# Optimization experiments

Measured on AMD Instinct MI355X. Metric: run time of the kernel, lower is better.

## Reference

```python
import jax, jax.numpy as jnp
import numpy as np

RGB2GRAY = jnp.array([0.299, 0.587, 0.114], dtype=jnp.float32)


def _trilinear_slice(grid, z, y, x):
    """grid: (F, L, GH, GW); z,y,x: (H, W) float positions in index space
    (align_corners=True convention). Returns (H, W, F)."""
    F_, L, GH, GW = grid.shape
    z = jnp.clip(z, 0.0, L - 1)
    y = jnp.clip(y, 0.0, GH - 1)
    x = jnp.clip(x, 0.0, GW - 1)
    z0 = jnp.floor(z).astype(jnp.int32); z1 = jnp.minimum(z0 + 1, L - 1)
    y0 = jnp.floor(y).astype(jnp.int32); y1 = jnp.minimum(y0 + 1, GH - 1)
    x0 = jnp.floor(x).astype(jnp.int32); x1 = jnp.minimum(x0 + 1, GW - 1)
    wz = (z - z0)[..., None]  # (H, W, 1)
    wy = (y - y0)[..., None]
    wx = (x - x0)[..., None]

    def g(zi, yi, xi):  # gather corner -> (H, W, F)
        return jnp.moveaxis(grid[:, zi, yi, xi], 0, -1)

    c00 = g(z0, y0, x0) * (1 - wx) + g(z0, y0, x1) * wx
    c01 = g(z0, y1, x0) * (1 - wx) + g(z0, y1, x1) * wx
    c10 = g(z1, y0, x0) * (1 - wx) + g(z1, y0, x1) * wx
    c11 = g(z1, y1, x0) * (1 - wx) + g(z1, y1, x1) * wx
    c0 = c00 * (1 - wy) + c01 * wy
    c1 = c10 * (1 - wy) + c11 * wy
    return c0 * (1 - wz) + c1 * wz


def setup_inputs() -> dict:
    key = jax.random.key(0)
    k = jax.random.split(key, 5)
    H, W = 1080, 1920
    N, F_, L, GH, GW = 50, 16, 8, 16, 16
    hidden = 64
    rgb = jax.random.uniform(k[0], (H, W, 3), dtype=jnp.float32)
    grids = jax.random.normal(k[1], (N, F_, L, GH, GW), dtype=jnp.float32) * 0.1
    W1 = jax.random.normal(k[2], (hidden, F_), dtype=jnp.float32) * (1.0 / np.sqrt(F_))
    W2 = jax.random.normal(k[3], (hidden, hidden), dtype=jnp.float32) * (1.0 / np.sqrt(hidden))
    W3 = jax.random.normal(k[4], (12, hidden), dtype=jnp.float32) * (1.0 / np.sqrt(hidden))
    return {"rgb": rgb, "grids": grids, "W1": W1, "W2": W2, "W3": W3, "cam_idx": 3}


def reference(rgb, grids, W1, W2, W3, cam_idx):
    H, W, _ = rgb.shape
    _, F_, L, GH, GW = grids.shape
    grid = grids[cam_idx]  # (F, L, GH, GW)
    # guidance: gray in [0,1]; grid_sample coords in [-1,1] with align_corners=True
    # map directly to index space: pos = coord01 * (size - 1)
    gray = jnp.clip(jnp.tensordot(rgb, RGB2GRAY, axes=([-1], [0])), 0.0, 1.0)  # (H, W)
    gy = jnp.linspace(0.0, 1.0, H, dtype=jnp.float32)[:, None]  # (H, 1)
    gx = jnp.linspace(0.0, 1.0, W, dtype=jnp.float32)[None, :]  # (1, W)
    z = gray * (L - 1)
    y = jnp.broadcast_to(gy * (GH - 1), (H, W))
    x = jnp.broadcast_to(gx * (GW - 1), (H, W))
    feat = _trilinear_slice(grid, z, y, x)  # (H, W, F)
    # tiny per-pixel MLP (bias-free, torch Linear applies x @ W.T)
    h = jnp.tanh(feat @ W1.T)
    h = jnp.tanh(h @ W2.T)
    out = h @ W3.T  # (H, W, 12)
    return out.reshape(1, H, W, 3, 4)
```

## Files before the change

### kernel.cpp

```cpp
#include <hip/hip_runtime.h>

#define H_IMG 1080
#define W_IMG 1920
#define NPIX (H_IMG * W_IMG)

typedef __attribute__((ext_vector_type(8))) short bfrag8;
typedef __attribute__((ext_vector_type(4))) float facc4;

#define PK2_OFF 131072
#define PK3_OFF 147456
#define PK1_OFF 151552

__device__ __forceinline__ void split_bf16(float x, unsigned short& hi, unsigned short& lo) {
    unsigned xu = __float_as_uint(x);
    hi = (unsigned short)(xu >> 16);
    float hif = __uint_as_float(xu & 0xffff0000u);
    float lof = x - hif;
    lo = (unsigned short)(__float_as_uint(lof) >> 16);
}

__global__ void prep_kernel(const float* __restrict__ grids,
                            const int* __restrict__ cam_idx,
                            const float* __restrict__ W1,
                            const float* __restrict__ W2,
                            const float* __restrict__ W3,
                            float* __restrict__ grid_t,
                            unsigned short* __restrict__ pk1,
                            unsigned short* __restrict__ pk2,
                            unsigned short* __restrict__ pk3) {
    int idx = blockIdx.x * 256 + threadIdx.x;
    {
        int f = idx & 15, x = (idx >> 4) & 15, y = (idx >> 8) & 15, z = (idx >> 12) & 7;
        int cam = cam_idx[0];
        grid_t[idx] = grids[(((cam * 16 + f) * 8 + z) * 16 + y) * 16 + x];
    }
    if (idx < 8192) {
        int i = idx & 7, lane = (idx >> 3) & 63, h = (idx >> 9) & 1,
            s = (idx >> 10) & 1, mt = (idx >> 11) & 3;
        int j = mt * 16 + (lane & 15);
        int k = s * 32 + (lane >> 4) * 8 + i;
        unsigned short hi, lo;
        split_bf16(W2[j * 64 + k], hi, lo);
        pk2[idx] = h ? lo : hi;
    } else if (idx < 10240) {
        int e = idx - 8192;
        int i = e & 7, lane = (e >> 3) & 63, h = (e >> 9) & 1, s = (e >> 10) & 1;
        int c = lane & 15;
        int k = s * 32 + (lane >> 4) * 8 + i;
        float x = (c < 12) ? W3[c * 64 + k] : 0.0f;
        unsigned short hi, lo;
        split_bf16(x, hi, lo);
        pk3[e] = h ? lo : hi;
    } else if (idx < 14336) {
        int e = idx - 10240;
        int i = e & 7, lane = (e >> 3) & 63, h = (e >> 9) & 1, mt = (e >> 10) & 3;
        int j = mt * 16 + (lane & 15);
        int k = (lane >> 4) * 8 + i;
        float x = (k < 16) ? W1[j * 16 + k] : 0.0f;
        unsigned short hi, lo;
        split_bf16(x, hi, lo);
        pk1[e] = h ? lo : hi;
    }
}

__device__ __forceinline__ float fast_tanh(float x) {
    float e = exp2f(x * 2.8853900817779268f);
    return 1.0f - 2.0f * __builtin_amdgcn_rcpf(e + 1.0f);
}

__device__ __forceinline__ unsigned pack_hi_pair(float e, float o) {
    return __builtin_amdgcn_perm(__float_as_uint(o), __float_as_uint(e), 0x07060302u);
}

#define DS_FENCE() asm volatile("s_waitcnt lgkmcnt(0)" ::: "memory")
#define MFMA16(A, B, C) __builtin_amdgcn_mfma_f32_16x16x32_bf16((A), (B), (C), 0, 0, 0)

__global__ __launch_bounds__(256, 3)
void nbat_main(const float* __restrict__ rgb,
               const float* __restrict__ grid_t,
               const unsigned short* __restrict__ pk1,
               const unsigned short* __restrict__ pk2,
               const unsigned short* __restrict__ pk3,
               float* __restrict__ out) {
    __shared__ __align__(16) unsigned hbuf[4][2048];

    const int tid = threadIdx.x;
    const int w = tid >> 6, l = tid & 63;
    const int g = l >> 4, cc = l & 15;
    unsigned* hb = hbuf[w];
    uint4* hb4 = (uint4*)hb;

    const int pixbase = blockIdx.x * 256 + w * 64;
    const int pix = pixbase + l;
    const int row = pix / W_IMG;
    const int col = pix - row * W_IMG;

    float r = rgb[3 * pix + 0];
    float gch = rgb[3 * pix + 1];
    float b = rgb[3 * pix + 2];
    float gray = fminf(fmaxf(0.299f * r + 0.587f * gch + 0.114f * b, 0.0f), 1.0f);

    float z = fminf(fmaxf(gray * 7.0f, 0.0f), 7.0f);
    float y = (float)row * (15.0f / 1079.0f);
    float x = (float)col * (15.0f / 1919.0f);

    float zf = floorf(z), yf = floorf(y), xf = floorf(x);
    int z0 = (int)zf, y0 = (int)yf, x0 = (int)xf;
    int z1 = min(z0 + 1, 7), y1 = min(y0 + 1, 15), x1 = min(x0 + 1, 15);
    float wz = z - zf, wy = y - yf, wx = x - xf;

    float feat[16];
#pragma unroll
    for (int i = 0; i < 16; ++i) feat[i] = 0.0f;

    const float4* gt4 = (const float4*)grid_t;
#pragma unroll
    for (int cz = 0; cz < 2; ++cz) {
        int zz = cz ? z1 : z0;
        float wwz = cz ? wz : (1.0f - wz);
#pragma unroll
        for (int cy = 0; cy < 2; ++cy) {
            int yy = cy ? y1 : y0;
            float wwzy = wwz * (cy ? wy : (1.0f - wy));
#pragma unroll
            for (int cx = 0; cx < 2; ++cx) {
                int xx = cx ? x1 : x0;
                float wc = wwzy * (cx ? wx : (1.0f - wx));
                int base = ((zz * 16 + yy) * 16 + xx) * 4;
#pragma unroll
                for (int q = 0; q < 4; ++q) {
                    float4 v = gt4[base + q];
                    feat[4 * q + 0] = fmaf(wc, v.x, feat[4 * q + 0]);
                    feat[4 * q + 1] = fmaf(wc, v.y, feat[4 * q + 1]);
                    feat[4 * q + 2] = fmaf(wc, v.z, feat[4 * q + 2]);
                    feat[4 * q + 3] = fmaf(wc, v.w, feat[4 * q + 3]);
                }
            }
        }
    }

    const int sl = (l >> 1) & 3;
    {
        uint4 q0, q1;
        q0.x = pack_hi_pair(feat[0], feat[1]);
        q0.y = pack_hi_pair(feat[2], feat[3]);
        q0.z = pack_hi_pair(feat[4], feat[5]);
        q0.w = pack_hi_pair(feat[6], feat[7]);
        q1.x = pack_hi_pair(feat[8], feat[9]);
        q1.y = pack_hi_pair(feat[10], feat[11]);
        q1.z = pack_hi_pair(feat[12], feat[13]);
        q1.w = pack_hi_pair(feat[14], feat[15]);
        uint4 zz4 = make_uint4(0u, 0u, 0u, 0u);
        hb4[l * 4 + (0 ^ sl)] = q0;
        hb4[l * 4 + (1 ^ sl)] = q1;
        hb4[l * 4 + (2 ^ sl)] = zz4;
        hb4[l * 4 + (3 ^ sl)] = zz4;
    }
    DS_FENCE();

    bfrag8 bf[4];
#pragma unroll
    for (int nt = 0; nt < 4; ++nt) {
        int p = cc + 16 * nt;
        bf[nt] = __builtin_bit_cast(bfrag8, hb4[p * 4 + (g ^ ((p >> 1) & 3))]);
    }
    DS_FENCE();

    auto transition = [&](const facc4& v, int mtl, int nt) __attribute__((always_inline)) {
        float t0 = fast_tanh(v[0]);
        float t1 = fast_tanh(v[1]);
        float t2 = fast_tanh(v[2]);
        float t3 = fast_tanh(v[3]);
        unsigned hA = pack_hi_pair(t0, t1);
        unsigned hB = pack_hi_pair(t2, t3);
        float l0 = t0 - __uint_as_float(hA << 16);
        float l1 = t1 - __uint_as_float(hA & 0xffff0000u);
        float l2 = t2 - __uint_as_float(hB << 16);
        float l3 = t3 - __uint_as_float(hB & 0xffff0000u);
        unsigned lA = pack_hi_pair(l0, l1);
        unsigned lB = pack_hi_pair(l2, l3);
        int p = cc + 16 * nt;
        int u = p * 16 + ((((mtl << 1) + (g >> 1)) ^ ((p >> 1) & 3)) << 2) + ((g & 1) << 1);
        *(uint2*)(hb + u) = make_uint2(hA, hB);
        *(uint2*)(hb + 1024 + u) = make_uint2(lA, lB);
    };

    const bfrag8* pk1v = (const bfrag8*)pk1;
    const bfrag8* pk2v = (const bfrag8*)pk2;

    facc4 acc2[4][4];
#pragma unroll
    for (int mt = 0; mt < 4; ++mt)
#pragma unroll
        for (int nt = 0; nt < 4; ++nt) acc2[mt][nt] = (facc4){0.f, 0.f, 0.f, 0.f};

#pragma unroll
    for (int s = 0; s < 2; ++s) {
        facc4 a1[2][4];
#pragma unroll
        for (int mtl = 0; mtl < 2; ++mtl)
#pragma unroll
            for (int nt = 0; nt < 4; ++nt) a1[mtl][nt] = (facc4){0.f, 0.f, 0.f, 0.f};
#pragma unroll
        for (int mtl = 0; mtl < 2; ++mtl) {
            int mt = 2 * s + mtl;
            bfrag8 w1h = pk1v[(mt * 2 + 0) * 64 + l];
            bfrag8 w1l = pk1v[(mt * 2 + 1) * 64 + l];
#pragma unroll
            for (int nt = 0; nt < 4; ++nt) {
                a1[mtl][nt] = MFMA16(w1l, bf[nt], a1[mtl][nt]);
                a1[mtl][nt] = MFMA16(w1h, bf[nt], a1[mtl][nt]);
            }
        }
#pragma unroll
        for (int mtl = 0; mtl < 2; ++mtl)
#pragma unroll
            for (int nt = 0; nt < 4; ++nt) transition(a1[mtl][nt], mtl, nt);
        DS_FENCE();
        bfrag8 w2h[4], w2l[4];
#pragma unroll
        for (int mt = 0; mt < 4; ++mt) {
            w2h[mt] = pk2v[((mt * 2 + s) * 2 + 0) * 64 + l];
            w2l[mt] = pk2v[((mt * 2 + s) * 2 + 1) * 64 + l];
        }
#pragma unroll
        for (int nt = 0; nt < 4; ++nt) {
            int p = cc + 16 * nt;
            int sw = (p >> 1) & 3;
            uint4 qh = hb4[p * 4 + (g ^ sw)];
            uint4 ql = hb4[256 + p * 4 + (g ^ sw)];
            bfrag8 bh = __builtin_bit_cast(bfrag8, qh);
            bfrag8 bl = __builtin_bit_cast(bfrag8, ql);
#pragma unroll
            for (int mt = 0; mt < 4; ++mt) {
                acc2[mt][nt] = MFMA16(w2h[mt], bl, acc2[mt][nt]);
                acc2[mt][nt] = MFMA16(w2l[mt], bh, acc2[mt][nt]);
                acc2[mt][nt] = MFMA16(w2h[mt], bh, acc2[mt][nt]);
            }
        }
        DS_FENCE();
    }

    const bfrag8* pk3v = (const bfrag8*)pk3;
    facc4 o3[4];
#pragma unroll
    for (int nt = 0; nt < 4; ++nt) o3[nt] = (facc4){0.f, 0.f, 0.f, 0.f};

#pragma unroll
    for (int s = 0; s < 2; ++s) {
#pragma unroll
        for (int mtl = 0; mtl < 2; ++mtl)
#pragma unroll
            for (int nt = 0; nt < 4; ++nt) transition(acc2[2 * s + mtl][nt], mtl, nt);
        DS_FENCE();
        bfrag8 w3h = pk3v[(s * 2 + 0) * 64 + l];
        bfrag8 w3l = pk3v[(s * 2 + 1) * 64 + l];
#pragma unroll
        for (int nt = 0; nt < 4; ++nt) {
            int p = cc + 16 * nt;
            int sw = (p >> 1) & 3;
            uint4 qh = hb4[p * 4 + (g ^ sw)];
            uint4 ql = hb4[256 + p * 4 + (g ^ sw)];
            bfrag8 bh = __builtin_bit_cast(bfrag8, qh);
            bfrag8 bl = __builtin_bit_cast(bfrag8, ql);
            o3[nt] = MFMA16(w3h, bl, o3[nt]);
            o3[nt] = MFMA16(w3l, bh, o3[nt]);
            o3[nt] = MFMA16(w3h, bh, o3[nt]);
        }
        if (s == 0) DS_FENCE();
    }

    if (g < 3) {
#pragma unroll
        for (int nt = 0; nt < 4; ++nt) {
            int p = pixbase + 16 * nt + cc;
            *(float4*)(out + p * 12 + 4 * g) =
                make_float4(o3[nt][0], o3[nt][1], o3[nt][2], o3[nt][3]);
        }
    }
}

extern "C" void kernel_launch(void* const* d_in, const int* in_sizes, int n_in,
                              void* d_out, int out_size, void* d_ws, size_t ws_size,
                              hipStream_t stream) {
    const float* rgb   = (const float*)d_in[0];
    const float* grids = (const float*)d_in[1];
    const float* W1    = (const float*)d_in[2];
    const float* W2    = (const float*)d_in[3];
    const float* W3    = (const float*)d_in[4];
    const int*   cam   = (const int*)d_in[5];

    float* grid_t = (float*)d_ws;
    unsigned short* pk2 = (unsigned short*)((char*)d_ws + PK2_OFF);
    unsigned short* pk3 = (unsigned short*)((char*)d_ws + PK3_OFF);
    unsigned short* pk1 = (unsigned short*)((char*)d_ws + PK1_OFF);

    hipLaunchKernelGGL(prep_kernel, dim3(128), dim3(256), 0, stream,
                       grids, cam, W1, W2, W3, grid_t, pk1, pk2, pk3);
    hipLaunchKernelGGL(nbat_main, dim3(NPIX / 256), dim3(256), 0, stream,
                       rgb, grid_t, pk1, pk2, pk3, (float*)d_out);
}
```

Baseline: 176.8 us.

## Drop hi/lo split of activations, round-to-nearest bf16, full-layer staging

Activations in layers 2 and 3 are now a single round-to-nearest bf16 value instead of a hi+lo bf16 pair. This cuts MFMAs per layer from 3 to 2 per tile and removes the low-part LDS traffic. Layer 1 is now computed in full before one transition, with the LDS swizzle simplified and the explicit lgkmcnt waits replaced by compiler-only barriers. The risks are lower numerical accuracy in the activations and possible LDS hazards if the compiler does not order the wave-local writes and reads, plus more live registers (acc1 and acc2 full arrays).

```diff
diff --git a/kernel.cpp b/kernel.cpp
--- a/kernel.cpp
+++ b/kernel.cpp
@@ -68,11 +68,13 @@
     return 1.0f - 2.0f * __builtin_amdgcn_rcpf(e + 1.0f);
 }
 
-__device__ __forceinline__ unsigned pack_hi_pair(float e, float o) {
-    return __builtin_amdgcn_perm(__float_as_uint(o), __float_as_uint(e), 0x07060302u);
-}
-
-#define DS_FENCE() asm volatile("s_waitcnt lgkmcnt(0)" ::: "memory")
+__device__ __forceinline__ unsigned rtn_pair(float e, float o) {
+    unsigned ue = __float_as_uint(e) + 0x8000u;
+    unsigned uo = __float_as_uint(o) + 0x8000u;
+    return __builtin_amdgcn_perm(uo, ue, 0x07060302u);
+}
+
+#define CBAR() asm volatile("" ::: "memory")
 #define MFMA16(A, B, C) __builtin_amdgcn_mfma_f32_16x16x32_bf16((A), (B), (C), 0, 0, 0)
 
 __global__ __launch_bounds__(256, 3)
@@ -139,135 +141,134 @@
         }
     }
 
-    const int sl = (l >> 1) & 3;
+    const int slw = l & 3;
     {
         uint4 q0, q1;
-        q0.x = pack_hi_pair(feat[0], feat[1]);
-        q0.y = pack_hi_pair(feat[2], feat[3]);
-        q0.z = pack_hi_pair(feat[4], feat[5]);
-        q0.w = pack_hi_pair(feat[6], feat[7]);
-        q1.x = pack_hi_pair(feat[8], feat[9]);
-        q1.y = pack_hi_pair(feat[10], feat[11]);
-        q1.z = pack_hi_pair(feat[12], feat[13]);
-        q1.w = pack_hi_pair(feat[14], feat[15]);
+        q0.x = rtn_pair(feat[0], feat[1]);
+        q0.y = rtn_pair(feat[2], feat[3]);
+        q0.z = rtn_pair(feat[4], feat[5]);
+        q0.w = rtn_pair(feat[6], feat[7]);
+        q1.x = rtn_pair(feat[8], feat[9]);
+        q1.y = rtn_pair(feat[10], feat[11]);
+        q1.z = rtn_pair(feat[12], feat[13]);
+        q1.w = rtn_pair(feat[14], feat[15]);
         uint4 zz4 = make_uint4(0u, 0u, 0u, 0u);
-        hb4[l * 4 + (0 ^ sl)] = q0;
-        hb4[l * 4 + (1 ^ sl)] = q1;
-        hb4[l * 4 + (2 ^ sl)] = zz4;
-        hb4[l * 4 + (3 ^ sl)] = zz4;
-    }
-    DS_FENCE();
+        hb4[l * 4 + (0 ^ slw)] = q0;
+        hb4[l * 4 + (1 ^ slw)] = q1;
+        hb4[l * 4 + (2 ^ slw)] = zz4;
+        hb4[l * 4 + (3 ^ slw)] = zz4;
+    }
+    CBAR();
 
     bfrag8 bf[4];
 #pragma unroll
     for (int nt = 0; nt < 4; ++nt) {
         int p = cc + 16 * nt;
-        bf[nt] = __builtin_bit_cast(bfrag8, hb4[p * 4 + (g ^ ((p >> 1) & 3))]);
-    }
-    DS_FENCE();
-
-    auto transition = [&](const facc4& v, int mtl, int nt) __attribute__((always_inline)) {
+        bf[nt] = __builtin_bit_cast(bfrag8, hb4[p * 4 + (g ^ (p & 3))]);
+    }
+    CBAR();
+
+    auto transition = [&](const facc4& v, int mt, int nt) __attribute__((always_inline)) {
         float t0 = fast_tanh(v[0]);
         float t1 = fast_tanh(v[1]);
         float t2 = fast_tanh(v[2]);
         float t3 = fast_tanh(v[3]);
-        unsigned hA = pack_hi_pair(t0, t1);
-        unsigned hB = pack_hi_pair(t2, t3);
-        float l0 = t0 - __uint_as_float(hA << 16);
-        float l1 = t1 - __uint_as_float(hA & 0xffff0000u);
-        float l2 = t2 - __uint_as_float(hB << 16);
-        float l3 = t3 - __uint_as_float(hB & 0xffff0000u);
-        unsigned lA = pack_hi_pair(l0, l1);
-        unsigned lB = pack_hi_pair(l2, l3);
+        unsigned A = rtn_pair(t0, t1);
+        unsigned B = rtn_pair(t2, t3);
         int p = cc + 16 * nt;
-        int u = p * 16 + ((((mtl << 1) + (g >> 1)) ^ ((p >> 1) & 3)) << 2) + ((g & 1) << 1);
-        *(uint2*)(hb + u) = make_uint2(hA, hB);
-        *(uint2*)(hb + 1024 + u) = make_uint2(lA, lB);
+        int mtl = mt & 1;
+        int c = 2 * mtl + (g >> 1);
+        int u = (mt >> 1) * 1024 + p * 16 + (((c ^ (p & 3)) << 2) + 2 * (g & 1));
+        *(uint2*)(hb + u) = make_uint2(A, B);
     };
 
     const bfrag8* pk1v = (const bfrag8*)pk1;
     const bfrag8* pk2v = (const bfrag8*)pk2;
-
+    const bfrag8* pk3v = (const bfrag8*)pk3;
+
+    facc4 acc1[4][4];
+#pragma unroll
+    for (int mt = 0; mt < 4; ++mt)
+#pragma unroll
+        for (int nt = 0; nt < 4; ++nt) acc1[mt][nt] = (facc4){0.f, 0.f, 0.f, 0.f};
+#pragma unroll
+    for (int mt = 0; mt < 4; ++mt) {
+        bfrag8 w1h = pk1v[(mt * 2 + 0) * 64 + l];
+        bfrag8 w1l = pk1v[(mt * 2 + 1) * 64 + l];
+#pragma unroll
+        for (int nt = 0; nt < 4; ++nt) {
+            acc1[mt][nt] = MFMA16(w1l, bf[nt], acc1[mt][nt]);
+            acc1[mt][nt] = MFMA16(w1h, bf[nt], acc1[mt][nt]);
+        }
+    }
+
+#pragma unroll
+    for (int mt = 0; mt < 4; ++mt)
+#pragma unroll
+        for (int nt = 0; nt < 4; ++nt) transition(acc1[mt][nt], mt, nt);
+    CBAR();
+
+    uint4 Bq[2][4];
+#pragma unroll
+    for (int s = 0; s < 2; ++s)
+#pragma unroll
+        for (int nt = 0; nt < 4; ++nt) {
+            int p = cc + 16 * nt;
+            Bq[s][nt] = hb4[s * 256 + p * 4 + (g ^ (p & 3))];
+        }
     facc4 acc2[4][4];
 #pragma unroll
     for (int mt = 0; mt < 4; ++mt)
 #pragma unroll
         for (int nt = 0; nt < 4; ++nt) acc2[mt][nt] = (facc4){0.f, 0.f, 0.f, 0.f};
-
-#pragma unroll
-    for (int s = 0; s < 2; ++s) {
-        facc4 a1[2][4];
-#pragma unroll
-        for (int mtl = 0; mtl < 2; ++mtl)
-#pragma unroll
-            for (int nt = 0; nt < 4; ++nt) a1[mtl][nt] = (facc4){0.f, 0.f, 0.f, 0.f};
-#pragma unroll
-        for (int mtl = 0; mtl < 2; ++mtl) {
-            int mt = 2 * s + mtl;
-            bfrag8 w1h = pk1v[(mt * 2 + 0) * 64 + l];
-            bfrag8 w1l = pk1v[(mt * 2 + 1) * 64 + l];
-#pragma unroll
-            for (int nt = 0; nt < 4; ++nt) {
-                a1[mtl][nt] = MFMA16(w1l, bf[nt], a1[mtl][nt]);
-                a1[mtl][nt] = MFMA16(w1h, bf[nt], a1[mtl][nt]);
-            }
-        }
-#pragma unroll
-        for (int mtl = 0; mtl < 2; ++mtl)
-#pragma unroll
-            for (int nt = 0; nt < 4; ++nt) transition(a1[mtl][nt], mtl, nt);
-        DS_FENCE();
-        bfrag8 w2h[4], w2l[4];
-#pragma unroll
-        for (int mt = 0; mt < 4; ++mt) {
-            w2h[mt] = pk2v[((mt * 2 + s) * 2 + 0) * 64 + l];
-            w2l[mt] = pk2v[((mt * 2 + s) * 2 + 1) * 64 + l];
-        }
+#pragma unroll
+    for (int mt = 0; mt < 4; ++mt) {
+        bfrag8 w2h0 = pk2v[((mt * 2 + 0) * 2 + 0) * 64 + l];
+        bfrag8 w2l0 = pk2v[((mt * 2 + 0) * 2 + 1) * 64 + l];
+        bfrag8 w2h1 = pk2v[((mt * 2 + 1) * 2 + 0) * 64 + l];
+        bfrag8 w2l1 = pk2v[((mt * 2 + 1) * 2 + 1) * 64 + l];
+#pragma unroll
+        for (int nt = 0; nt < 4; ++nt) {
+            bfrag8 b0 = __builtin_bit_cast(bfrag8, Bq[0][nt]);
+            bfrag8 b1 = __builtin_bit_cast(bfrag8, Bq[1][nt]);
+            acc2[mt][nt] = MFMA16(w2l0, b0, acc2[mt][nt]);
+            acc2[mt][nt] = MFMA16(w2h0, b0, acc2[mt][nt]);
+            acc2[mt][nt] = MFMA16(w2l1, b1, acc2[mt][nt]);
+            acc2[mt][nt] = MFMA16(w2h1, b1, acc2[mt][nt]);
+        }
+    }
+    CBAR();
+
+#pragma unroll
+    for (int mt = 0; mt < 4; ++mt)
+#pragma unroll
+        for (int nt = 0; nt < 4; ++nt) transition(acc2[mt][nt], mt, nt);
+    CBAR();
+
+#pragma unroll
+    for (int s = 0; s < 2; ++s)
 #pragma unroll
         for (int nt = 0; nt < 4; ++nt) {
             int p = cc + 16 * nt;
-            int sw = (p >> 1) & 3;
-            uint4 qh = hb4[p * 4 + (g ^ sw)];
-            uint4 ql = hb4[256 + p * 4 + (g ^ sw)];
-            bfrag8 bh = __builtin_bit_cast(bfrag8, qh);
-            bfrag8 bl = __builtin_bit_cast(bfrag8, ql);
-#pragma unroll
-            for (int mt = 0; mt < 4; ++mt) {
-                acc2[mt][nt] = MFMA16(w2h[mt], bl, acc2[mt][nt]);
-                acc2[mt][nt] = MFMA16(w2l[mt], bh, acc2[mt][nt]);
-                acc2[mt][nt] = MFMA16(w2h[mt], bh, acc2[mt][nt]);
-            }
-        }
-        DS_FENCE();
-    }
-
-    const bfrag8* pk3v = (const bfrag8*)pk3;
+            Bq[s][nt] = hb4[s * 256 + p * 4 + (g ^ (p & 3))];
+        }
     facc4 o3[4];
 #pragma unroll
     for (int nt = 0; nt < 4; ++nt) o3[nt] = (facc4){0.f, 0.f, 0.f, 0.f};
-
-#pragma unroll
-    for (int s = 0; s < 2; ++s) {
-#pragma unroll
-        for (int mtl = 0; mtl < 2; ++mtl)
-#pragma unroll
-            for (int nt = 0; nt < 4; ++nt) transition(acc2[2 * s + mtl][nt], mtl, nt);
-        DS_FENCE();
-        bfrag8 w3h = pk3v[(s * 2 + 0) * 64 + l];
-        bfrag8 w3l = pk3v[(s * 2 + 1) * 64 + l];
-#pragma unroll
-        for (int nt = 0; nt < 4; ++nt) {
-            int p = cc + 16 * nt;
-            int sw = (p >> 1) & 3;
-            uint4 qh = hb4[p * 4 + (g ^ sw)];
-            uint4 ql = hb4[256 + p * 4 + (g ^ sw)];
-            bfrag8 bh = __builtin_bit_cast(bfrag8, qh);
-            bfrag8 bl = __builtin_bit_cast(bfrag8, ql);
-            o3[nt] = MFMA16(w3h, bl, o3[nt]);
-            o3[nt] = MFMA16(w3l, bh, o3[nt]);
-            o3[nt] = MFMA16(w3h, bh, o3[nt]);
-        }
-        if (s == 0) DS_FENCE();
+    {
+        bfrag8 w3h0 = pk3v[0 * 64 + l];
+        bfrag8 w3l0 = pk3v[1 * 64 + l];
+        bfrag8 w3h1 = pk3v[2 * 64 + l];
+        bfrag8 w3l1 = pk3v[3 * 64 + l];
+#pragma unroll
+        for (int nt = 0; nt < 4; ++nt) {
+            bfrag8 b0 = __builtin_bit_cast(bfrag8, Bq[0][nt]);
+            bfrag8 b1 = __builtin_bit_cast(bfrag8, Bq[1][nt]);
+            o3[nt] = MFMA16(w3l0, b0, o3[nt]);
+            o3[nt] = MFMA16(w3h0, b0, o3[nt]);
+            o3[nt] = MFMA16(w3l1, b1, o3[nt]);
+            o3[nt] = MFMA16(w3h1, b1, o3[nt]);
+        }
     }
 
     if (g < 3) {
```

Measured after the change: 191.0 us. 1.08x slower.
